# Performance work log

Hardware: AMD Instinct MI355X
Metric: run time of the kernel (lower is better)

Reference implementation:

```python
import jax, jax.numpy as jnp
import numpy as np

N, E, F, H, C, L = 50000, 800000, 32, 4, 32, 3
HC = H * C
NEG = 0.2  # leaky_relu negative slope (GATv2Conv default and explicit LeakyReLU(0.2))


def _gat_layer(x, src, dst, ea, Wl, bl, Wr, br, att, We, cb, lW, lb, bsc, bsh):
    # GATv2 linear transforms: [N, F] -> [N, H, C]
    xl = (x @ Wl + bl).reshape(N, H, C)
    xr = (x @ Wr + br).reshape(N, H, C)
    xj = xl[src]            # [E, H, C] messages from source nodes
    xi = xr[dst]            # [E, H, C] target-side features
    ep = (ea[:, None] @ We).reshape(E, H, C)  # edge-linear, edge_dim=1
    e = jax.nn.leaky_relu(xi + xj + ep, NEG)
    logits = jnp.einsum('ehc,hc->eh', e, att)            # [E, H]
    # segment softmax over destination node neighborhoods
    m = jax.ops.segment_max(logits, dst, num_segments=N)
    a = jnp.exp(logits - m[dst])
    denom = jax.ops.segment_sum(a, dst, num_segments=N)
    alpha = a / denom[dst]                               # [E, H]
    msg = xj * alpha[..., None]                          # [E, H, C]
    out = jax.ops.segment_sum(msg, dst, num_segments=N).reshape(N, HC) + cb
    # trailing per-layer MLP: Linear -> LeakyReLU(0.2) -> BatchNorm1d (eval, affine)
    h = jax.nn.leaky_relu(out @ lW + lb, NEG)
    return h * bsc + bsh


def setup_inputs() -> dict:
    key = jax.random.key(0)
    ks = jax.random.split(key, 24)
    s = 0.1
    inp = {
        'x': jax.random.normal(ks[0], (N, F), jnp.float32),
        'edge_index': jax.random.randint(ks[1], (2, E), 0, N, jnp.int32),
        'edge_attr': jax.random.normal(ks[2], (E,), jnp.float32),
        'batch': jnp.zeros((N,), jnp.int32),
        # stacked per-layer conv params (all 3 layers share shapes: F==hidden)
        'Wl': jax.random.normal(ks[3], (L, F, HC), jnp.float32) * s,
        'bl': jnp.zeros((L, HC), jnp.float32),
        'Wr': jax.random.normal(ks[4], (L, F, HC), jnp.float32) * s,
        'br': jnp.zeros((L, HC), jnp.float32),
        'att': jax.random.normal(ks[5], (L, H, C), jnp.float32) * s,
        'We': jax.random.normal(ks[6], (L, 1, HC), jnp.float32) * s,
        'conv_b': jnp.zeros((L, HC), jnp.float32),
        'lin_W': jax.random.normal(ks[7], (L, HC, F), jnp.float32) * s,
        'lin_b': jnp.zeros((L, F), jnp.float32),
        'bn_scale': jnp.ones((L, F), jnp.float32),
        'bn_shift': jnp.zeros((L, F), jnp.float32),
        # fcn head: hidden -> 256 -> 32 -> num_classes
        'W1': jax.random.normal(ks[8], (F, 256), jnp.float32) * s,
        'b1': jnp.zeros((256,), jnp.float32),
        'W2': jax.random.normal(ks[9], (256, 32), jnp.float32) * s,
        'b2': jnp.zeros((32,), jnp.float32),
        'W3': jax.random.normal(ks[10], (32, 2), jnp.float32) * s,
        'b3': jnp.zeros((2,), jnp.float32),
    }
    return inp


def reference(x, edge_index, edge_attr, batch, Wl, bl, Wr, br, att, We, conv_b,
              lin_W, lin_b, bn_scale, bn_shift, W1, b1, W2, b2, W3, b3):
    src, dst = edge_index[0], edge_index[1]
    ea = jnp.abs(edge_attr)
    h = x
    for i in range(L):
        h = _gat_layer(h, src, dst, ea, Wl[i], bl[i], Wr[i], br[i], att[i],
                       We[i], conv_b[i], lin_W[i], lin_b[i], bn_scale[i], bn_shift[i])
    # global mean pool over graphs in batch (single graph here, B=1)
    B = 1
    sums = jax.ops.segment_sum(h, batch, num_segments=B)
    cnts = jax.ops.segment_sum(jnp.ones((N, 1), h.dtype), batch, num_segments=B)
    g = sums / cnts
    g = jax.nn.leaky_relu(g @ W1 + b1, NEG)
    g = jax.nn.leaky_relu(g @ W2 + b2, NEG)
    return g @ W3 + b3
```

## Files before the change

kernel.cpp:

```cpp
#include <hip/hip_runtime.h>
#include <hip/hip_bf16.h>
#include <math.h>

#define NN 50000
#define EE 800000
#define HC 128
#define FF 32
#define NEG 0.2f
#define CAP 64
#define LOG2E 1.4426950408889634f


__global__ void k_bucket(const int* __restrict__ src, const int* __restrict__ dst,
                         const float* __restrict__ ea, int* __restrict__ cnt,
                         int2* __restrict__ pairs) {
    int e = blockIdx.x * 256 + threadIdx.x;
    if (e >= EE) return;
    int d = dst[e];
    int pos = atomicAdd(&cnt[d], 1);
    pairs[d * CAP + pos] = make_int2(src[e], __float_as_int(fabsf(ea[e])));
}


__global__ void k_hist(const int* __restrict__ dst, int* __restrict__ deg) {
    int e = blockIdx.x * 256 + threadIdx.x;
    if (e < EE) atomicAdd(&deg[dst[e]], 1);
}

__global__ void k_scan1(const int* __restrict__ deg, int* __restrict__ part) {
    __shared__ int sd[256];
    int b = blockIdx.x, t = threadIdx.x;
    int base = b * 1024 + t * 4;
    int s = 0;
#pragma unroll
    for (int i = 0; i < 4; ++i) { int idx = base + i; if (idx < NN) s += deg[idx]; }
    sd[t] = s; __syncthreads();
    for (int off = 128; off; off >>= 1) { if (t < off) sd[t] += sd[t + off]; __syncthreads(); }
    if (t == 0) part[b] = sd[0];
}

__global__ void k_scan2(int* __restrict__ part, int nb) {
    if (threadIdx.x == 0) {
        int run = 0;
        for (int i = 0; i < nb; ++i) { int v = part[i]; part[i] = run; run += v; }
    }
}

__global__ void k_scan3(const int* __restrict__ deg, const int* __restrict__ part,
                        int* __restrict__ rowptr) {
    __shared__ int sd[256];
    int b = blockIdx.x, t = threadIdx.x;
    int base = b * 1024 + t * 4;
    int v[4]; int mine = 0;
#pragma unroll
    for (int i = 0; i < 4; ++i) { int idx = base + i; v[i] = (idx < NN) ? deg[idx] : 0; mine += v[i]; }
    sd[t] = mine; __syncthreads();
    for (int off = 1; off < 256; off <<= 1) {
        int tmp = (t >= off) ? sd[t - off] : 0;
        __syncthreads();
        sd[t] += tmp;
        __syncthreads();
    }
    int run = sd[t] - mine + part[b];
#pragma unroll
    for (int i = 0; i < 4; ++i) { int idx = base + i; if (idx < NN) rowptr[idx] = run; run += v[i]; }
    if (b == 0 && t == 0) rowptr[NN] = EE;
}

__global__ void k_scatter(const int* __restrict__ src, const int* __restrict__ dst,
                          const float* __restrict__ ea, const int* __restrict__ rowptr,
                          int* __restrict__ fill, int2* __restrict__ pairs) {
    int e = blockIdx.x * 256 + threadIdx.x;
    if (e >= EE) return;
    int d = dst[e];
    int pos = rowptr[d] + atomicAdd(&fill[d], 1);
    pairs[pos] = make_int2(src[e], __float_as_int(fabsf(ea[e])));
}


__global__ __launch_bounds__(256) void k_dual_linear(
        const float* __restrict__ x,
        const float* __restrict__ Wl, const float* __restrict__ bl,
        const float* __restrict__ Wr, const float* __restrict__ br,
        float* __restrict__ xl, float* __restrict__ xr) {
    const int t = threadIdx.x;
    const int l = t & 63;
    const int half = l >> 5;
    const int lc = l & 31;
    const float* __restrict__ W  = half ? Wr : Wl;
    const float* __restrict__ bb = half ? br : bl;
    float* __restrict__ outp     = half ? xr : xl;

    float4 w[32];
#pragma unroll
    for (int k = 0; k < 32; ++k)
        w[k] = *(const float4*)(W + k * 128 + 4 * lc);
    const float4 bias = *(const float4*)(bb + 4 * lc);

    const int gw = blockIdx.x * 4 + (t >> 6);
    const int nW = gridDim.x * 4;
    const int q8 = 4 * (l & 7);

    int n = gw;
    if (n >= NN) return;
    float4 r0 = *(const float4*)(x + (size_t)n * 32 + q8);
    int n1 = n + nW < NN ? n + nW : n;
    float4 r1 = *(const float4*)(x + (size_t)n1 * 32 + q8);

    for (; n < NN; n += nW) {
        float4 cur = r0;
        r0 = r1;
        int np = n + 2 * nW < NN ? n + 2 * nW : n;
        r1 = *(const float4*)(x + (size_t)np * 32 + q8);

        float4 acc = bias;
#pragma unroll
        for (int q = 0; q < 8; ++q) {
            float vx = __shfl(cur.x, q, 8);
            float vy = __shfl(cur.y, q, 8);
            float vz = __shfl(cur.z, q, 8);
            float vw = __shfl(cur.w, q, 8);
            acc.x = fmaf(vx, w[4 * q + 0].x, acc.x);
            acc.y = fmaf(vx, w[4 * q + 0].y, acc.y);
            acc.z = fmaf(vx, w[4 * q + 0].z, acc.z);
            acc.w = fmaf(vx, w[4 * q + 0].w, acc.w);
            acc.x = fmaf(vy, w[4 * q + 1].x, acc.x);
            acc.y = fmaf(vy, w[4 * q + 1].y, acc.y);
            acc.z = fmaf(vy, w[4 * q + 1].z, acc.z);
            acc.w = fmaf(vy, w[4 * q + 1].w, acc.w);
            acc.x = fmaf(vz, w[4 * q + 2].x, acc.x);
            acc.y = fmaf(vz, w[4 * q + 2].y, acc.y);
            acc.z = fmaf(vz, w[4 * q + 2].z, acc.z);
            acc.w = fmaf(vz, w[4 * q + 2].w, acc.w);
            acc.x = fmaf(vw, w[4 * q + 3].x, acc.x);
            acc.y = fmaf(vw, w[4 * q + 3].y, acc.y);
            acc.z = fmaf(vw, w[4 * q + 3].z, acc.z);
            acc.w = fmaf(vw, w[4 * q + 3].w, acc.w);
        }
        *(float4*)(outp + (size_t)n * 128 + 4 * lc) = acc;
    }
}


template<bool BUCKET, bool LAST>
__global__ __launch_bounds__(256) void k_gat_mlp(
        const float* __restrict__ xl, const float* __restrict__ xr,
        const int* __restrict__ idx,
        const int2* __restrict__ pairs,
        const float* __restrict__ att,
        const float* __restrict__ Wev,
        const float* __restrict__ cb,
        const float* __restrict__ lW,
        const float* __restrict__ lb,
        const float* __restrict__ bsc, const float* __restrict__ bsh,
        float* __restrict__ hout,
        float* __restrict__ part_g) {
    __shared__ float sW[HC * FF];
    __shared__ float gp[FF];
    {
        float4* d4 = (float4*)sW;
        const float4* s4 = (const float4*)lW;
        for (int i = threadIdx.x; i < HC * FF / 4; i += 256) d4[i] = s4[i];
        if (LAST && threadIdx.x < 32) gp[threadIdx.x] = 0.f;
    }
    __syncthreads();

    const int l = threadIdx.x & 31;
    const int n = blockIdx.x * 8 + (threadIdx.x >> 5);
    const char* __restrict__ xlp = (const char*)xl + (l << 4);

    float4 att4 = ((const float4*)att)[l];
    att4.x *= LOG2E; att4.y *= LOG2E; att4.z *= LOG2E; att4.w *= LOG2E;
    float4 we4  = ((const float4*)Wev)[l];
    float4 xr4  = ((const float4*)xr)[n * 32 + l];
    int beg, end;
    if (BUCKET) { beg = n * CAP; end = beg + idx[n]; }
    else        { beg = idx[n];  end = idx[n + 1]; }
    const int last = end - 1;

    float m = -INFINITY, s = 0.f;
    float4 acc = make_float4(0.f, 0.f, 0.f, 0.f);

    if (beg < end) {
        int2 p0 = pairs[beg];
        int2 p1 = pairs[beg + 1 < last ? beg + 1 : last];
        int2 p2 = pairs[beg + 2 < last ? beg + 2 : last];
        float4 x0 = *(const float4*)(xlp + (p0.x << 9));
        float4 x1 = *(const float4*)(xlp + (p1.x << 9));

#pragma unroll 2
        for (int j = beg; j <= last; ++j) {
            int jn = j + 3 < last ? j + 3 : last;
            int2 pn = pairs[jn];
            float4 xn = *(const float4*)(xlp + (p2.x << 9));

            float sea = __int_as_float(p0.y);
            float4 v;
            v.x = fmaf(sea, we4.x, xr4.x + x0.x);
            v.y = fmaf(sea, we4.y, xr4.y + x0.y);
            v.z = fmaf(sea, we4.z, xr4.z + x0.z);
            v.w = fmaf(sea, we4.w, xr4.w + x0.w);
            v.x = fmaxf(v.x, NEG * v.x);
            v.y = fmaxf(v.y, NEG * v.y);
            v.z = fmaxf(v.z, NEG * v.z);
            v.w = fmaxf(v.w, NEG * v.w);
            float pl = v.x * att4.x;
            pl = fmaf(v.y, att4.y, pl);
            pl = fmaf(v.z, att4.z, pl);
            pl = fmaf(v.w, att4.w, pl);
            pl += __shfl_xor(pl, 4);
            pl += __shfl_xor(pl, 2);
            pl += __shfl_xor(pl, 1);

            float mn = fmaxf(m, pl);
            float d  = __builtin_amdgcn_exp2f(fminf(m, pl) - mn);
            bool up  = pl > m;
            float c  = up ? d : 1.0f;
            float e  = up ? 1.0f : d;
            s = fmaf(s, c, e);
            acc.x = fmaf(acc.x, c, e * x0.x);
            acc.y = fmaf(acc.y, c, e * x0.y);
            acc.z = fmaf(acc.z, c, e * x0.z);
            acc.w = fmaf(acc.w, c, e * x0.w);
            m = mn;

            p0 = p1; p1 = p2; p2 = pn;
            x0 = x1; x1 = xn;
        }
    }

    float inv = (s > 0.f) ? 1.f / s : 0.f;
    float4 cb4 = ((const float4*)cb)[l];
    float4 o;
    o.x = fmaf(acc.x, inv, cb4.x);
    o.y = fmaf(acc.y, inv, cb4.y);
    o.z = fmaf(acc.z, inv, cb4.z);
    o.w = fmaf(acc.w, inv, cb4.w);

    const int cg = (l >> 2) & 7;
    const int kg = l & 3;
    const int kg8 = kg * 8;
    float4 a2 = (kg == 0) ? *(const float4*)(lb + 4 * cg)
                          : make_float4(0.f, 0.f, 0.f, 0.f);
#pragma unroll
    for (int j = 0; j < 8; ++j) {
        float vx = __shfl(o.x, kg8 + j, 32);
        float vy = __shfl(o.y, kg8 + j, 32);
        float vz = __shfl(o.z, kg8 + j, 32);
        float vw = __shfl(o.w, kg8 + j, 32);
        const float* wp = sW + (32 * kg + 4 * j) * 32 + 4 * cg;
        float4 w0 = *(const float4*)(wp);
        float4 w1 = *(const float4*)(wp + 32);
        float4 w2 = *(const float4*)(wp + 64);
        float4 w3 = *(const float4*)(wp + 96);
        a2.x = fmaf(vx, w0.x, a2.x); a2.y = fmaf(vx, w0.y, a2.y);
        a2.z = fmaf(vx, w0.z, a2.z); a2.w = fmaf(vx, w0.w, a2.w);
        a2.x = fmaf(vy, w1.x, a2.x); a2.y = fmaf(vy, w1.y, a2.y);
        a2.z = fmaf(vy, w1.z, a2.z); a2.w = fmaf(vy, w1.w, a2.w);
        a2.x = fmaf(vz, w2.x, a2.x); a2.y = fmaf(vz, w2.y, a2.y);
        a2.z = fmaf(vz, w2.z, a2.z); a2.w = fmaf(vz, w2.w, a2.w);
        a2.x = fmaf(vw, w3.x, a2.x); a2.y = fmaf(vw, w3.y, a2.y);
        a2.z = fmaf(vw, w3.z, a2.z); a2.w = fmaf(vw, w3.w, a2.w);
    }
    a2.x += __shfl_xor(a2.x, 1); a2.x += __shfl_xor(a2.x, 2);
    a2.y += __shfl_xor(a2.y, 1); a2.y += __shfl_xor(a2.y, 2);
    a2.z += __shfl_xor(a2.z, 1); a2.z += __shfl_xor(a2.z, 2);
    a2.w += __shfl_xor(a2.w, 1); a2.w += __shfl_xor(a2.w, 2);

    if (kg == 0) {
        const float4 sc4 = *(const float4*)(bsc + 4 * cg);
        const float4 sh4 = *(const float4*)(bsh + 4 * cg);
        float4 hq;
        hq.x = fmaxf(a2.x, NEG * a2.x);
        hq.y = fmaxf(a2.y, NEG * a2.y);
        hq.z = fmaxf(a2.z, NEG * a2.z);
        hq.w = fmaxf(a2.w, NEG * a2.w);
        hq.x = fmaf(hq.x, sc4.x, sh4.x);
        hq.y = fmaf(hq.y, sc4.y, sh4.y);
        hq.z = fmaf(hq.z, sc4.z, sh4.z);
        hq.w = fmaf(hq.w, sc4.w, sh4.w);
        if (LAST) {
            atomicAdd(&gp[4 * cg + 0], hq.x);
            atomicAdd(&gp[4 * cg + 1], hq.y);
            atomicAdd(&gp[4 * cg + 2], hq.z);
            atomicAdd(&gp[4 * cg + 3], hq.w);
        } else {
            *(float4*)(hout + (size_t)n * 32 + 4 * cg) = hq;
        }
    }
    if (LAST) {
        __syncthreads();
        if (threadIdx.x < 32)
            atomicAdd(&part_g[(blockIdx.x & 63) * 32 + threadIdx.x], gp[threadIdx.x]);
    }
}


__global__ void k_head(const float* __restrict__ part_g,
                       const float* __restrict__ W1, const float* __restrict__ b1,
                       const float* __restrict__ W2, const float* __restrict__ b2,
                       const float* __restrict__ W3, const float* __restrict__ b3,
                       float* __restrict__ out) {
    __shared__ float red[256];
    __shared__ float gv[32];
    __shared__ float h1[256];
    __shared__ float h2[32];
    int t = threadIdx.x;
    int col = t & 31, r = t >> 5;
    float lsum = 0.f;
#pragma unroll
    for (int k = 0; k < 8; ++k) lsum += part_g[(r + 8 * k) * 32 + col];
    red[t] = lsum; __syncthreads();
    if (r < 4) red[t] += red[t + 128];
    __syncthreads();
    if (r < 2) red[t] += red[t + 64];
    __syncthreads();
    if (r < 1) gv[col] = (red[t] + red[t + 32]) * (1.0f / NN);
    __syncthreads();
    float acc = b1[t];
#pragma unroll 8
    for (int k = 0; k < 32; ++k) acc += gv[k] * W1[k * 256 + t];
    h1[t] = acc > 0.f ? acc : NEG * acc;
    __syncthreads();
    if (t < 32) {
        float a = b2[t];
        for (int k = 0; k < 256; ++k) a += h1[k] * W2[k * 32 + t];
        h2[t] = a > 0.f ? a : NEG * a;
    }
    __syncthreads();
    if (t < 2) {
        float a = b3[t];
#pragma unroll
        for (int k = 0; k < 32; ++k) a += h2[k] * W3[k * 2 + t];
        out[t] = a;
    }
}


static inline size_t alignup(size_t x) { return (x + 255) & ~size_t(255); }

extern "C" void kernel_launch(void* const* d_in, const int* in_sizes, int n_in,
                              void* d_out, int out_size, void* d_ws, size_t ws_size,
                              hipStream_t stream) {
    const float* x     = (const float*)d_in[0];
    const int*   eidx  = (const int*)d_in[1];
    const float* eattr = (const float*)d_in[2];
    const float* Wl    = (const float*)d_in[4];
    const float* bl    = (const float*)d_in[5];
    const float* Wr    = (const float*)d_in[6];
    const float* br    = (const float*)d_in[7];
    const float* att   = (const float*)d_in[8];
    const float* We    = (const float*)d_in[9];
    const float* cb    = (const float*)d_in[10];
    const float* lW    = (const float*)d_in[11];
    const float* lb    = (const float*)d_in[12];
    const float* bsc   = (const float*)d_in[13];
    const float* bsh   = (const float*)d_in[14];
    const float* W1    = (const float*)d_in[15];
    const float* b1    = (const float*)d_in[16];
    const float* W2    = (const float*)d_in[17];
    const float* b2    = (const float*)d_in[18];
    const float* W3    = (const float*)d_in[19];
    const float* b3    = (const float*)d_in[20];

    const int* srcp = eidx;
    const int* dstp = eidx + EE;

    char* ws = (char*)d_ws;
    size_t off = 0;
    float* xl = (float*)(ws + off); off += alignup((size_t)NN * HC * 4);
    float* xr = (float*)(ws + off); off += alignup((size_t)NN * HC * 4);
    float* hA = (float*)(ws + off); off += alignup((size_t)NN * FF * 4);
    float* hB = (float*)(ws + off); off += alignup((size_t)NN * FF * 4);

    size_t boff = off;
    int2*  pairsB = (int2*) (ws + boff); boff += alignup((size_t)NN * CAP * 8);
    int*   cntB   = (int*)  (ws + boff); size_t z0 = boff; boff += alignup((size_t)NN * 4);
    float* partGB = (float*)(ws + boff); boff += alignup(64 * 32 * 4);
    const size_t zlenB = boff - z0;
    const bool bucket = (ws_size >= boff);

    const float* cur = x;
    float* hbuf[2] = {hA, hB};

    if (bucket) {
        hipMemsetAsync(cntB, 0, zlenB, stream);
        k_bucket<<<(EE + 255) / 256, 256, 0, stream>>>(srcp, dstp, eattr, cntB, pairsB);
        for (int i = 0; i < 3; ++i) {
            k_dual_linear<<<768, 256, 0, stream>>>(cur, Wl + i * FF * HC, bl + i * HC,
                                                   Wr + i * FF * HC, br + i * HC, xl, xr);
            if (i < 2)
                k_gat_mlp<true, false><<<NN / 8, 256, 0, stream>>>(
                    xl, xr, cntB, pairsB, att + i * HC, We + i * HC, cb + i * HC,
                    lW + i * HC * FF, lb + i * FF, bsc + i * FF, bsh + i * FF,
                    hbuf[i & 1], partGB);
            else
                k_gat_mlp<true, true><<<NN / 8, 256, 0, stream>>>(
                    xl, xr, cntB, pairsB, att + i * HC, We + i * HC, cb + i * HC,
                    lW + i * HC * FF, lb + i * FF, bsc + i * FF, bsh + i * FF,
                    hbuf[i & 1], partGB);
            cur = hbuf[i & 1];
        }
        k_head<<<1, 256, 0, stream>>>(partGB, W1, b1, W2, b2, W3, b3, (float*)d_out);
    } else {
        size_t coff = off;
        int2*  pairsC = (int2*) (ws + coff); coff += alignup((size_t)EE * 8);
        int*   rowptr = (int*)  (ws + coff); coff += alignup((size_t)(NN + 1) * 4);
        int*   deg    = (int*)  (ws + coff); size_t z1 = coff; coff += alignup((size_t)NN * 4);
        int*   fill   = (int*)  (ws + coff); coff += alignup((size_t)NN * 4);
        int*   part   = (int*)  (ws + coff); coff += alignup(64 * 4);
        float* partGC = (float*)(ws + coff); coff += alignup(64 * 32 * 4);
        const size_t zlenC = coff - z1;

        hipMemsetAsync(deg, 0, zlenC, stream);
        const int nChunk = (NN + 1023) / 1024;
        k_hist<<<(EE + 255) / 256, 256, 0, stream>>>(dstp, deg);
        k_scan1<<<nChunk, 256, 0, stream>>>(deg, part);
        k_scan2<<<1, 64, 0, stream>>>(part, nChunk);
        k_scan3<<<nChunk, 256, 0, stream>>>(deg, part, rowptr);
        k_scatter<<<(EE + 255) / 256, 256, 0, stream>>>(srcp, dstp, eattr, rowptr, fill, pairsC);

        for (int i = 0; i < 3; ++i) {
            k_dual_linear<<<768, 256, 0, stream>>>(cur, Wl + i * FF * HC, bl + i * HC,
                                                   Wr + i * FF * HC, br + i * HC, xl, xr);
            if (i < 2)
                k_gat_mlp<false, false><<<NN / 8, 256, 0, stream>>>(
                    xl, xr, rowptr, pairsC, att + i * HC, We + i * HC, cb + i * HC,
                    lW + i * HC * FF, lb + i * FF, bsc + i * FF, bsh + i * FF,
                    hbuf[i & 1], partGC);
            else
                k_gat_mlp<false, true><<<NN / 8, 256, 0, stream>>>(
                    xl, xr, rowptr, pairsC, att + i * HC, We + i * HC, cb + i * HC,
                    lW + i * HC * FF, lb + i * FF, bsc + i * FF, bsh + i * FF,
                    hbuf[i & 1], partGC);
            cur = hbuf[i & 1];
        }
        k_head<<<1, 256, 0, stream>>>(partGC, W1, b1, W2, b2, W3, b3, (float*)d_out);
    }
}
```

Baseline: 465.6 us.

## Fuse edge bucketing with first dual linear and drop LDS weight staging

Merges the edge-bucketing kernel and the first layer's dual linear transform into one launch split by block range, so the two independent stages overlap. The dual linear now handles four nodes per wave and streams weights from cache instead of holding all 32 float4 weights in registers. The GAT+MLP kernel reads the MLP weights directly from global memory rather than staging them in shared memory, removing a per-block copy and barrier. In exchange, weight reads now depend on cache hits, which adds load traffic.

```diff
diff --git a/kernel.cpp b/kernel.cpp
--- a/kernel.cpp
+++ b/kernel.cpp
@@ -9,16 +9,97 @@
 #define NEG 0.2f
 #define CAP 64
 #define LOG2E 1.4426950408889634f
-
-
-__global__ void k_bucket(const int* __restrict__ src, const int* __restrict__ dst,
-                         const float* __restrict__ ea, int* __restrict__ cnt,
-                         int2* __restrict__ pairs) {
-    int e = blockIdx.x * 256 + threadIdx.x;
-    if (e >= EE) return;
-    int d = dst[e];
-    int pos = atomicAdd(&cnt[d], 1);
-    pairs[d * CAP + pos] = make_int2(src[e], __float_as_int(fabsf(ea[e])));
+#define DUALB 784
+
+__device__ __forceinline__ void fma4(float4& a, float s, const float4& w) {
+    a.x = fmaf(s, w.x, a.x);
+    a.y = fmaf(s, w.y, a.y);
+    a.z = fmaf(s, w.z, a.z);
+    a.w = fmaf(s, w.w, a.w);
+}
+
+
+__device__ __forceinline__ void dual_work(
+        int bid, int nblocks, int t,
+        const float* __restrict__ x,
+        const float* __restrict__ Wl, const float* __restrict__ bl,
+        const float* __restrict__ Wr, const float* __restrict__ br,
+        float* __restrict__ xl, float* __restrict__ xr) {
+    const int l = t & 63;
+    const int half = l >> 5;
+    const int lc = l & 31;
+    const float* __restrict__ W  = half ? Wr : Wl;
+    const float* __restrict__ bb = half ? br : bl;
+    float* __restrict__ outp     = half ? xr : xl;
+    const float4 bias = *(const float4*)(bb + 4 * lc);
+
+    const int wv = bid * 4 + (t >> 6);
+    const int nW = nblocks * 4;
+    const int q8 = 4 * (l & 7);
+
+    for (int n0 = wv * 4; n0 < NN; n0 += nW * 4) {
+        float4 c0 = *(const float4*)(x + (size_t)n0 * 32 + q8);
+        float4 c1 = *(const float4*)(x + (size_t)(n0 + 1) * 32 + q8);
+        float4 c2 = *(const float4*)(x + (size_t)(n0 + 2) * 32 + q8);
+        float4 c3 = *(const float4*)(x + (size_t)(n0 + 3) * 32 + q8);
+        float4 a0 = bias, a1 = bias, a2 = bias, a3 = bias;
+#pragma unroll
+        for (int q = 0; q < 8; ++q) {
+            float4 w0 = *(const float4*)(W + (4 * q + 0) * 128 + 4 * lc);
+            float4 w1 = *(const float4*)(W + (4 * q + 1) * 128 + 4 * lc);
+            float4 w2 = *(const float4*)(W + (4 * q + 2) * 128 + 4 * lc);
+            float4 w3 = *(const float4*)(W + (4 * q + 3) * 128 + 4 * lc);
+            float s;
+            s = __shfl(c0.x, q, 8); fma4(a0, s, w0);
+            s = __shfl(c0.y, q, 8); fma4(a0, s, w1);
+            s = __shfl(c0.z, q, 8); fma4(a0, s, w2);
+            s = __shfl(c0.w, q, 8); fma4(a0, s, w3);
+            s = __shfl(c1.x, q, 8); fma4(a1, s, w0);
+            s = __shfl(c1.y, q, 8); fma4(a1, s, w1);
+            s = __shfl(c1.z, q, 8); fma4(a1, s, w2);
+            s = __shfl(c1.w, q, 8); fma4(a1, s, w3);
+            s = __shfl(c2.x, q, 8); fma4(a2, s, w0);
+            s = __shfl(c2.y, q, 8); fma4(a2, s, w1);
+            s = __shfl(c2.z, q, 8); fma4(a2, s, w2);
+            s = __shfl(c2.w, q, 8); fma4(a2, s, w3);
+            s = __shfl(c3.x, q, 8); fma4(a3, s, w0);
+            s = __shfl(c3.y, q, 8); fma4(a3, s, w1);
+            s = __shfl(c3.z, q, 8); fma4(a3, s, w2);
+            s = __shfl(c3.w, q, 8); fma4(a3, s, w3);
+        }
+        *(float4*)(outp + (size_t)n0 * 128 + 4 * lc) = a0;
+        *(float4*)(outp + (size_t)(n0 + 1) * 128 + 4 * lc) = a1;
+        *(float4*)(outp + (size_t)(n0 + 2) * 128 + 4 * lc) = a2;
+        *(float4*)(outp + (size_t)(n0 + 3) * 128 + 4 * lc) = a3;
+    }
+}
+
+__global__ __launch_bounds__(256) void k_dual(
+        const float* __restrict__ x,
+        const float* __restrict__ Wl, const float* __restrict__ bl,
+        const float* __restrict__ Wr, const float* __restrict__ br,
+        float* __restrict__ xl, float* __restrict__ xr) {
+    dual_work(blockIdx.x, gridDim.x, threadIdx.x, x, Wl, bl, Wr, br, xl, xr);
+}
+
+__global__ __launch_bounds__(256) void k_pre(
+        const float* __restrict__ x,
+        const float* __restrict__ Wl, const float* __restrict__ bl,
+        const float* __restrict__ Wr, const float* __restrict__ br,
+        float* __restrict__ xl, float* __restrict__ xr,
+        const int* __restrict__ src, const int* __restrict__ dst,
+        const float* __restrict__ ea, int* __restrict__ cnt,
+        int2* __restrict__ pairs) {
+    if (blockIdx.x < DUALB) {
+        dual_work(blockIdx.x, DUALB, threadIdx.x, x, Wl, bl, Wr, br, xl, xr);
+    } else {
+        int e = (blockIdx.x - DUALB) * 256 + threadIdx.x;
+        if (e < EE) {
+            int d = dst[e];
+            int pos = atomicAdd(&cnt[d], 1);
+            pairs[d * CAP + pos] = make_int2(src[e], __float_as_int(fabsf(ea[e])));
+        }
+    }
 }
 
 
@@ -75,70 +156,6 @@
     int d = dst[e];
     int pos = rowptr[d] + atomicAdd(&fill[d], 1);
     pairs[pos] = make_int2(src[e], __float_as_int(fabsf(ea[e])));
-}
-
-
-__global__ __launch_bounds__(256) void k_dual_linear(
-        const float* __restrict__ x,
-        const float* __restrict__ Wl, const float* __restrict__ bl,
-        const float* __restrict__ Wr, const float* __restrict__ br,
-        float* __restrict__ xl, float* __restrict__ xr) {
-    const int t = threadIdx.x;
-    const int l = t & 63;
-    const int half = l >> 5;
-    const int lc = l & 31;
-    const float* __restrict__ W  = half ? Wr : Wl;
-    const float* __restrict__ bb = half ? br : bl;
-    float* __restrict__ outp     = half ? xr : xl;
-
-    float4 w[32];
-#pragma unroll
-    for (int k = 0; k < 32; ++k)
-        w[k] = *(const float4*)(W + k * 128 + 4 * lc);
-    const float4 bias = *(const float4*)(bb + 4 * lc);
-
-    const int gw = blockIdx.x * 4 + (t >> 6);
-    const int nW = gridDim.x * 4;
-    const int q8 = 4 * (l & 7);
-
-    int n = gw;
-    if (n >= NN) return;
-    float4 r0 = *(const float4*)(x + (size_t)n * 32 + q8);
-    int n1 = n + nW < NN ? n + nW : n;
-    float4 r1 = *(const float4*)(x + (size_t)n1 * 32 + q8);
-
-    for (; n < NN; n += nW) {
-        float4 cur = r0;
-        r0 = r1;
-        int np = n + 2 * nW < NN ? n + 2 * nW : n;
-        r1 = *(const float4*)(x + (size_t)np * 32 + q8);
-
-        float4 acc = bias;
-#pragma unroll
-        for (int q = 0; q < 8; ++q) {
-            float vx = __shfl(cur.x, q, 8);
-            float vy = __shfl(cur.y, q, 8);
-            float vz = __shfl(cur.z, q, 8);
-            float vw = __shfl(cur.w, q, 8);
-            acc.x = fmaf(vx, w[4 * q + 0].x, acc.x);
-            acc.y = fmaf(vx, w[4 * q + 0].y, acc.y);
-            acc.z = fmaf(vx, w[4 * q + 0].z, acc.z);
-            acc.w = fmaf(vx, w[4 * q + 0].w, acc.w);
-            acc.x = fmaf(vy, w[4 * q + 1].x, acc.x);
-            acc.y = fmaf(vy, w[4 * q + 1].y, acc.y);
-            acc.z = fmaf(vy, w[4 * q + 1].z, acc.z);
-            acc.w = fmaf(vy, w[4 * q + 1].w, acc.w);
-            acc.x = fmaf(vz, w[4 * q + 2].x, acc.x);
-            acc.y = fmaf(vz, w[4 * q + 2].y, acc.y);
-            acc.z = fmaf(vz, w[4 * q + 2].z, acc.z);
-            acc.w = fmaf(vz, w[4 * q + 2].w, acc.w);
-            acc.x = fmaf(vw, w[4 * q + 3].x, acc.x);
-            acc.y = fmaf(vw, w[4 * q + 3].y, acc.y);
-            acc.z = fmaf(vw, w[4 * q + 3].z, acc.z);
-            acc.w = fmaf(vw, w[4 * q + 3].w, acc.w);
-        }
-        *(float4*)(outp + (size_t)n * 128 + 4 * lc) = acc;
-    }
 }
 
 
@@ -155,15 +172,11 @@
         const float* __restrict__ bsc, const float* __restrict__ bsh,
         float* __restrict__ hout,
         float* __restrict__ part_g) {
-    __shared__ float sW[HC * FF];
     __shared__ float gp[FF];
-    {
-        float4* d4 = (float4*)sW;
-        const float4* s4 = (const float4*)lW;
-        for (int i = threadIdx.x; i < HC * FF / 4; i += 256) d4[i] = s4[i];
-        if (LAST && threadIdx.x < 32) gp[threadIdx.x] = 0.f;
-    }
-    __syncthreads();
+    if (LAST) {
+        if (threadIdx.x < 32) gp[threadIdx.x] = 0.f;
+        __syncthreads();
+    }
 
     const int l = threadIdx.x & 31;
     const int n = blockIdx.x * 8 + (threadIdx.x >> 5);
@@ -242,25 +255,21 @@
     const int kg8 = kg * 8;
     float4 a2 = (kg == 0) ? *(const float4*)(lb + 4 * cg)
                           : make_float4(0.f, 0.f, 0.f, 0.f);
-#pragma unroll
+#pragma unroll 2
     for (int j = 0; j < 8; ++j) {
         float vx = __shfl(o.x, kg8 + j, 32);
         float vy = __shfl(o.y, kg8 + j, 32);
         float vz = __shfl(o.z, kg8 + j, 32);
         float vw = __shfl(o.w, kg8 + j, 32);
-        const float* wp = sW + (32 * kg + 4 * j) * 32 + 4 * cg;
+        const float* wp = lW + (32 * kg + 4 * j) * 32 + 4 * cg;
         float4 w0 = *(const float4*)(wp);
         float4 w1 = *(const float4*)(wp + 32);
         float4 w2 = *(const float4*)(wp + 64);
         float4 w3 = *(const float4*)(wp + 96);
-        a2.x = fmaf(vx, w0.x, a2.x); a2.y = fmaf(vx, w0.y, a2.y);
-        a2.z = fmaf(vx, w0.z, a2.z); a2.w = fmaf(vx, w0.w, a2.w);
-        a2.x = fmaf(vy, w1.x, a2.x); a2.y = fmaf(vy, w1.y, a2.y);
-        a2.z = fmaf(vy, w1.z, a2.z); a2.w = fmaf(vy, w1.w, a2.w);
-        a2.x = fmaf(vz, w2.x, a2.x); a2.y = fmaf(vz, w2.y, a2.y);
-        a2.z = fmaf(vz, w2.z, a2.z); a2.w = fmaf(vz, w2.w, a2.w);
-        a2.x = fmaf(vw, w3.x, a2.x); a2.y = fmaf(vw, w3.y, a2.y);
-        a2.z = fmaf(vw, w3.z, a2.z); a2.w = fmaf(vw, w3.w, a2.w);
+        fma4(a2, vx, w0);
+        fma4(a2, vy, w1);
+        fma4(a2, vz, w2);
+        fma4(a2, vw, w3);
     }
     a2.x += __shfl_xor(a2.x, 1); a2.x += __shfl_xor(a2.x, 2);
     a2.y += __shfl_xor(a2.y, 1); a2.y += __shfl_xor(a2.y, 2);
@@ -385,10 +394,13 @@
 
     if (bucket) {
         hipMemsetAsync(cntB, 0, zlenB, stream);
-        k_bucket<<<(EE + 255) / 256, 256, 0, stream>>>(srcp, dstp, eattr, cntB, pairsB);
+        const int bucketBlocks = (EE + 255) / 256;
+        k_pre<<<DUALB + bucketBlocks, 256, 0, stream>>>(
+            x, Wl, bl, Wr, br, xl, xr, srcp, dstp, eattr, cntB, pairsB);
         for (int i = 0; i < 3; ++i) {
-            k_dual_linear<<<768, 256, 0, stream>>>(cur, Wl + i * FF * HC, bl + i * HC,
-                                                   Wr + i * FF * HC, br + i * HC, xl, xr);
+            if (i > 0)
+                k_dual<<<DUALB, 256, 0, stream>>>(cur, Wl + i * FF * HC, bl + i * HC,
+                                                  Wr + i * FF * HC, br + i * HC, xl, xr);
             if (i < 2)
                 k_gat_mlp<true, false><<<NN / 8, 256, 0, stream>>>(
                     xl, xr, cntB, pairsB, att + i * HC, We + i * HC, cb + i * HC,
@@ -421,8 +433,8 @@
         k_scatter<<<(EE + 255) / 256, 256, 0, stream>>>(srcp, dstp, eattr, rowptr, fill, pairsC);
 
         for (int i = 0; i < 3; ++i) {
-            k_dual_linear<<<768, 256, 0, stream>>>(cur, Wl + i * FF * HC, bl + i * HC,
-                                                   Wr + i * FF * HC, br + i * HC, xl, xr);
+            k_dual<<<DUALB, 256, 0, stream>>>(cur, Wl + i * FF * HC, bl + i * HC,
+                                              Wr + i * FF * HC, br + i * HC, xl, xr);
             if (i < 2)
                 k_gat_mlp<false, false><<<NN / 8, 256, 0, stream>>>(
                     xl, xr, rowptr, pairsC, att + i * HC, We + i * HC, cb + i * HC,
```

New measurement: 653.1 us. 40.3% more time.
